# Kernel tuning notes

Measured on AMD Instinct MI355X. Metric: run time of the kernel, lower is better.

Reference implementation:

```python
import jax, jax.numpy as jnp
import numpy as np

N_NODES = 100000
N_TYPES = 7
N_EDGES = 400000
D = 128


def setup_inputs() -> dict:
    key = jax.random.key(0)
    k1, k2, k3, k4 = jax.random.split(key, 4)
    x = jax.random.normal(k1, (N_NODES, D), dtype=jnp.float32)
    edge_indices = jax.random.randint(k2, (N_TYPES, 2, N_EDGES), 0, N_NODES, dtype=jnp.int64)
    # per-type linear weights of the cloned base GNNs (scaled for stability)
    W = jax.random.normal(k3, (N_TYPES, D, D), dtype=jnp.float32) * (1.0 / np.sqrt(D))
    b = jax.random.normal(k4, (N_TYPES, D), dtype=jnp.float32) * 0.02
    return {"x": x, "edge_indices": edge_indices, "W": W, "b": b}


def _type_conv(x, src, dst, Wt, bt, n_nodes):
    # gather -> segment-mean aggregate -> linear, one edge type
    msg = x[src]                                                   # [E, D]
    summed = jax.ops.segment_sum(msg, dst, num_segments=n_nodes)   # [N, D]
    cnt = jax.ops.segment_sum(jnp.ones(src.shape, x.dtype), dst, num_segments=n_nodes)
    mean = summed / jnp.maximum(cnt, 1.0)[:, None]
    return mean @ Wt + bt


def reference(x, edge_indices, W, b):
    n_nodes = x.shape[0]
    n_types = edge_indices.shape[0]
    # loop over the small fixed set of edge types (structurally distinct GNNs)
    acc = jnp.zeros_like(x)
    for t in range(n_types):
        acc = acc + _type_conv(x, edge_indices[t, 0], edge_indices[t, 1], W[t], b[t], n_nodes)
    return acc / n_types
```

## Files before the change

### kernel.cpp

```cpp
#include <hip/hip_runtime.h>

#define N_NODES 100000
#define N_TYPES 7
#define N_EDGES 400000
#define DIM 128
#define NTOT (N_TYPES * N_NODES)
#define ETOT (N_TYPES * N_EDGES)

#define RBITS 10
#define RNODE 1024
#define NBUCK 98
#define NTB (N_TYPES * NBUCK)
#define BSTRIDE 128
#define CAP 6144
#define CHUNK 2048
#define NCHUNKS ((N_EDGES + CHUNK - 1) / CHUNK)

typedef short v8s __attribute__((ext_vector_type(8)));
typedef float v4f __attribute__((ext_vector_type(4)));

__device__ __forceinline__ unsigned short f2bf(float f) {
    unsigned int x = __float_as_uint(f);
    return (unsigned short)((x + 0x7FFFu + ((x >> 16) & 1u)) >> 16);
}

__global__ __launch_bounds__(256) void cast_x_kernel(
    const float* __restrict__ x, unsigned short* __restrict__ xb)
{
    int i = blockIdx.x * 256 + threadIdx.x;
    if (i >= N_NODES * DIM / 4) return;
    float4 v = reinterpret_cast<const float4*>(x)[i];
    ushort4 o;
    o.x = f2bf(v.x); o.y = f2bf(v.y); o.z = f2bf(v.z); o.w = f2bf(v.w);
    reinterpret_cast<ushort4*>(xb)[i] = o;
}

__global__ __launch_bounds__(256) void cast_wt_bsum_kernel(
    const float* __restrict__ W, const float* __restrict__ b,
    unsigned short* __restrict__ WT, float* __restrict__ bsum)
{
    if (blockIdx.x == 448) {
        int j = threadIdx.x;
        if (j < DIM) {
            float s = 0.f;
            for (int t = 0; t < N_TYPES; ++t) s += b[t * DIM + j];
            bsum[j] = s;
        }
        return;
    }
    int i = blockIdx.x * 256 + threadIdx.x;
    if (i >= N_TYPES * DIM * DIM) return;
    int t = i >> 14, r = i & 16383, j = r >> 7, k = r & 127;
    WT[i] = f2bf(W[(t << 14) + (k << 7) + j]);
}

__global__ __launch_bounds__(256) void binpass_kernel(
    const int* __restrict__ ei, int* __restrict__ gcur,
    unsigned int* __restrict__ bucketbuf)
{
    __shared__ unsigned int packedLds[CHUNK];
    __shared__ unsigned char bLds[CHUNK];
    __shared__ unsigned int sortedLds[CHUNK];
    __shared__ int cnt[BSTRIDE];
    __shared__ int lofs[BSTRIDE];
    __shared__ int gbase[BSTRIDE];

    const int blk = blockIdx.x;
    const int t = blk / NCHUNKS;
    const int c = blk - t * NCHUNKS;
    const int* srcp = ei + (size_t)t * 2 * N_EDGES;
    const int* dstp = srcp + N_EDGES;
    const int e0 = c * CHUNK;
    const int e1 = min(e0 + CHUNK, N_EDGES);
    const int tid = threadIdx.x;

    if (tid < BSTRIDE) cnt[tid] = 0;
    __syncthreads();

#pragma unroll
    for (int k = 0; k < CHUNK / 256; ++k) {
        int j = tid + k * 256;
        int e = e0 + j;
        unsigned char b = 0xFF;
        unsigned int pk = 0;
        if (e < e1) {
            int s = srcp[e];
            int d = dstp[e];
            b = (unsigned char)(d >> RBITS);
            pk = ((unsigned int)(d & (RNODE - 1)) << 17) | (unsigned int)s;
            atomicAdd(&cnt[b], 1);
        }
        packedLds[j] = pk;
        bLds[j] = b;
    }
    __syncthreads();

    if (tid < BSTRIDE) lofs[tid] = cnt[tid];
    __syncthreads();
    for (int off = 1; off < BSTRIDE; off <<= 1) {
        int tv = 0;
        if (tid >= off && tid < BSTRIDE) tv = lofs[tid - off];
        __syncthreads();
        if (tid < BSTRIDE) lofs[tid] += tv;
        __syncthreads();
    }
    if (tid < BSTRIDE) lofs[tid] -= cnt[tid];
    __syncthreads();

    if (tid < BSTRIDE) {
        int n = cnt[tid];
        int base = -1;
        if (n > 0 && tid < NBUCK) {
            int rel = atomicAdd(&gcur[t * BSTRIDE + tid], n);
            base = (t * BSTRIDE + tid) * CAP + rel;
        }
        gbase[tid] = base;
        cnt[tid] = lofs[tid];
    }
    __syncthreads();

#pragma unroll
    for (int k = 0; k < CHUNK / 256; ++k) {
        int j = tid + k * 256;
        unsigned char b = bLds[j];
        if (b != 0xFF) {
            int p = atomicAdd(&cnt[b], 1);
            sortedLds[p] = packedLds[j];
        }
    }
    __syncthreads();

    const int wave = tid >> 6, lane = tid & 63;
    for (int b = wave * 32; b < wave * 32 + 32; ++b) {
        if (b >= NBUCK) break;
        int base = gbase[b];
        if (base < 0) continue;
        int o = lofs[b];
        int n = cnt[b] - o;
        for (int i = lane; i < n; i += 64)
            bucketbuf[(size_t)base + i] = sortedLds[o + i];
    }
}

__global__ __launch_bounds__(1024) void bucket_base_kernel(
    const int* __restrict__ gcur, int* __restrict__ sbase, int* __restrict__ offs)
{
    __shared__ int s[1024];
    int tid = threadIdx.x;
    int v = 0;
    if (tid < NTB) {
        int t = tid / NBUCK, b = tid - t * NBUCK;
        v = min(gcur[t * BSTRIDE + b], CAP);
    }
    s[tid] = v;
    __syncthreads();
    for (int off = 1; off < 1024; off <<= 1) {
        int t2 = (tid >= off) ? s[tid - off] : 0;
        __syncthreads();
        s[tid] += t2;
        __syncthreads();
    }
    if (tid < NTB) sbase[tid] = s[tid] - v;
    if (tid == 0) offs[NTOT] = ETOT;
}

__global__ __launch_bounds__(256) void hist_place_kernel(
    const unsigned int* __restrict__ bucketbuf, const int* __restrict__ gcur,
    const int* __restrict__ sbase,
    int* __restrict__ offs, int* __restrict__ srcperm)
{
    __shared__ unsigned int sorted[CAP];
    __shared__ unsigned int sorted2[CAP];
    __shared__ int cnt[RNODE];
    __shared__ int s[256];

    const int blk = blockIdx.x;
    const int t = blk / NBUCK;
    const int b = blk - t * NBUCK;
    const int n = min(gcur[t * BSTRIDE + b], CAP);
    const int ebase = sbase[blk];
    const int g0 = b << RBITS;
    const int validR = min(RNODE, N_NODES - g0);
    const int tid = threadIdx.x;

    const unsigned int* bb = bucketbuf + (size_t)(t * BSTRIDE + b) * CAP;
    for (int i = tid; i < n; i += 256) sorted[i] = bb[i];
    for (int j = tid; j < RNODE; j += 256) cnt[j] = 0;
    __syncthreads();

    for (int i = tid; i < n; i += 256)
        atomicAdd(&cnt[sorted[i] >> 17], 1);
    __syncthreads();

    int base4 = tid * 4;
    int v[4], tot = 0;
#pragma unroll
    for (int k = 0; k < 4; ++k) { v[k] = cnt[base4 + k]; tot += v[k]; }
    s[tid] = tot;
    __syncthreads();
    for (int off = 1; off < 256; off <<= 1) {
        int t2 = (tid >= off) ? s[tid - off] : 0;
        __syncthreads();
        s[tid] += t2;
        __syncthreads();
    }
    int run = s[tid] - tot;
    int* og = offs + (size_t)t * N_NODES + g0;
#pragma unroll
    for (int k = 0; k < 4; ++k) {
        if (base4 + k < validR) og[base4 + k] = ebase + run;
        cnt[base4 + k] = run;
        run += v[k];
    }
    __syncthreads();

    for (int i = tid; i < n; i += 256) {
        unsigned int pk = sorted[i];
        int p = atomicAdd(&cnt[pk >> 17], 1);
        sorted2[p] = pk & 0x1FFFFu;
    }
    __syncthreads();

    int* outp = srcperm + ebase;
    for (int i = tid; i < n; i += 256) outp[i] = (int)sorted2[i];
}

__global__ __launch_bounds__(256) void aggregate_kernel(
    const unsigned short* __restrict__ xb,
    const int* __restrict__ offs,
    const int* __restrict__ srcperm,
    unsigned short* __restrict__ meanout,
    int grp0, int ngrp)
{
    int gi = blockIdx.x * 16 + (threadIdx.x >> 4);
    if (gi >= ngrp) return;
    int grp = grp0 + gi;
    int l = threadIdx.x & 15;

    int beg = offs[grp];
    int end = offs[grp + 1];
    int m = end - beg;

    int mm = m;
    mm = max(mm, __shfl_xor(mm, 16));
    mm = max(mm, __shfl_xor(mm, 32));

    float a[8];
#pragma unroll
    for (int j = 0; j < 8; ++j) a[j] = 0.f;

    const int eSafe = min(beg, ETOT - 1);
#pragma unroll 4
    for (int i = 0; i < mm; ++i) {
        bool valid = i < m;
        int e = valid ? (beg + i) : eSafe;
        int s = srcperm[e];
        uint4 v = *reinterpret_cast<const uint4*>(
            reinterpret_cast<const char*>(xb) + ((size_t)s << 8) + (l << 4));
        float w = valid ? 1.f : 0.f;
        a[0] += w * __uint_as_float(v.x << 16);
        a[1] += w * __uint_as_float(v.x & 0xFFFF0000u);
        a[2] += w * __uint_as_float(v.y << 16);
        a[3] += w * __uint_as_float(v.y & 0xFFFF0000u);
        a[4] += w * __uint_as_float(v.z << 16);
        a[5] += w * __uint_as_float(v.z & 0xFFFF0000u);
        a[6] += w * __uint_as_float(v.w << 16);
        a[7] += w * __uint_as_float(v.w & 0xFFFF0000u);
    }

    float inv = 1.0f / fmaxf((float)m, 1.0f);
    unsigned int p0, p1, p2, p3;
    asm("v_cvt_pk_bf16_f32 %0, %1, %2" : "=v"(p0) : "v"(a[0] * inv), "v"(a[1] * inv));
    asm("v_cvt_pk_bf16_f32 %0, %1, %2" : "=v"(p1) : "v"(a[2] * inv), "v"(a[3] * inv));
    asm("v_cvt_pk_bf16_f32 %0, %1, %2" : "=v"(p2) : "v"(a[4] * inv), "v"(a[5] * inv));
    asm("v_cvt_pk_bf16_f32 %0, %1, %2" : "=v"(p3) : "v"(a[6] * inv), "v"(a[7] * inv));
    uint4 o = make_uint4(p0, p1, p2, p3);
    *reinterpret_cast<uint4*>(
        reinterpret_cast<char*>(meanout) + ((size_t)gi << 8) + (l << 4)) = o;
}

__global__ __launch_bounds__(256) void matmul_kernel(
    const unsigned short* __restrict__ meanall, size_t meanStride,
    int t0, int nt,
    const unsigned short* __restrict__ WT,
    const float* __restrict__ bsum,
    float* __restrict__ out, int accum)
{
    __shared__ unsigned short sB[DIM * DIM];

    const int tid = threadIdx.x;
    const int wave = tid >> 6;
    const int lane = tid & 63;
    const int rlo = lane & 15;
    const int khi = lane >> 4;
    const int row0 = blockIdx.x * 128 + wave * 16;

    v4f acc[2][8];
#pragma unroll
    for (int u = 0; u < 2; ++u)
#pragma unroll
        for (int n = 0; n < 8; ++n) acc[u][n] = (v4f){0.f, 0.f, 0.f, 0.f};

    int rowA0 = row0 + rlo;       if (rowA0 >= N_NODES) rowA0 = N_NODES - 1;
    int rowA1 = row0 + 64 + rlo;  if (rowA1 >= N_NODES) rowA1 = N_NODES - 1;

    for (int tt = 0; tt < nt; ++tt) {
        int t = t0 + tt;
        __syncthreads();
        const uint4* gw = reinterpret_cast<const uint4*>(WT + ((size_t)t << 14));
#pragma unroll
        for (int i = 0; i < 8; ++i) {
            int c = tid + (i << 8);
            uint4 v = gw[c];
            int L = c << 4;
            int row = L >> 8;
            int sb = (row << 8) | ((L & 255) ^ ((row & 7) << 4));
            *reinterpret_cast<uint4*>(reinterpret_cast<char*>(sB) + sb) = v;
        }
        __syncthreads();

        const unsigned short* ar0 = meanall + (size_t)tt * meanStride + ((size_t)rowA0 << 7);
        const unsigned short* ar1 = meanall + (size_t)tt * meanStride + ((size_t)rowA1 << 7);

#pragma unroll
        for (int k0 = 0; k0 < DIM; k0 += 32) {
            v8s a0 = *reinterpret_cast<const v8s*>(ar0 + k0 + (khi << 3));
            v8s a1 = *reinterpret_cast<const v8s*>(ar1 + k0 + (khi << 3));
#pragma unroll
            for (int n = 0; n < 8; ++n) {
                int jrow = (n << 4) | rlo;
                int kb = (k0 + (khi << 3)) << 1;
                int sb = (jrow << 8) | (kb ^ ((jrow & 7) << 4));
                v8s bf = *reinterpret_cast<const v8s*>(reinterpret_cast<char*>(sB) + sb);
                acc[0][n] = __builtin_amdgcn_mfma_f32_16x16x32_bf16(a0, bf, acc[0][n], 0, 0, 0);
                acc[1][n] = __builtin_amdgcn_mfma_f32_16x16x32_bf16(a1, bf, acc[1][n], 0, 0, 0);
            }
        }
    }

    const float inv7 = 1.0f / 7.0f;
#pragma unroll
    for (int u = 0; u < 2; ++u) {
#pragma unroll
        for (int n = 0; n < 8; ++n) {
            int col = (n << 4) | rlo;
            float bs = bsum[col];
#pragma unroll
            for (int r = 0; r < 4; ++r) {
                int row = row0 + u * 64 + (khi << 2) + r;
                if (row < N_NODES) {
                    float* p = out + ((size_t)row << 7) + col;
                    if (accum) *p += acc[u][n][r] * inv7;
                    else       *p = (acc[u][n][r] + bs) * inv7;
                }
            }
        }
    }
}

__global__ __launch_bounds__(256) void out_init_kernel(
    const float* __restrict__ bsum, float* __restrict__ out)
{
    int i = blockIdx.x * 256 + threadIdx.x;
    if (i >= N_NODES * DIM / 4) return;
    int c4 = (i & 31) * 4;
    const float inv7 = 1.0f / 7.0f;
    float4 bv = *reinterpret_cast<const float4*>(bsum + c4);
    float4 o = make_float4(bv.x * inv7, bv.y * inv7, bv.z * inv7, bv.w * inv7);
    reinterpret_cast<float4*>(out)[i] = o;
}

extern "C" void kernel_launch(void* const* d_in, const int* in_sizes, int n_in,
                              void* d_out, int out_size, void* d_ws, size_t ws_size,
                              hipStream_t stream) {
    const float* x  = (const float*)d_in[0];
    const int*   ei = (const int*)d_in[1];
    const float* W  = (const float*)d_in[2];
    const float* b  = (const float*)d_in[3];
    float* out = (float*)d_out;

    char* p = (char*)d_ws;
    unsigned short* xb = (unsigned short*)p;          p += (size_t)N_NODES * DIM * 2;
    unsigned short* WT = (unsigned short*)p;          p += (size_t)N_TYPES * DIM * DIM * 2;
    float* bsum = (float*)p;                          p += 512;
    int* srcperm = (int*)p;                           p += (size_t)ETOT * 4;
    int* offs = (int*)p;                              p += (size_t)(NTOT + 1) * 4;
    int* sbase = (int*)p;                             p += 1024 * 4;
    int* gcur = (int*)p;                              p += (size_t)N_TYPES * BSTRIDE * 4;
    p = (char*)(((uintptr_t)p + 15) & ~(uintptr_t)15);
    unsigned int* bucketbuf = (unsigned int*)p;
    unsigned short* meanbuf = (unsigned short*)p;
    size_t mean1_bytes = (size_t)N_NODES * DIM * 2;
    size_t used = (size_t)(p - (char*)d_ws);
    size_t bucket_bytes = (size_t)N_TYPES * BSTRIDE * CAP * 4;
    bool fused = (ws_size >= used + 7 * mean1_bytes) &&
                 (7 * mean1_bytes >= bucket_bytes);

    cast_x_kernel<<<(N_NODES * DIM / 4 + 255) / 256, 256, 0, stream>>>(x, xb);
    cast_wt_bsum_kernel<<<449, 256, 0, stream>>>(W, b, WT, bsum);

    hipMemsetAsync(gcur, 0, (size_t)N_TYPES * BSTRIDE * 4, stream);
    binpass_kernel<<<N_TYPES * NCHUNKS, 256, 0, stream>>>(ei, gcur, bucketbuf);
    bucket_base_kernel<<<1, 1024, 0, stream>>>(gcur, sbase, offs);
    hist_place_kernel<<<NTB, 256, 0, stream>>>(bucketbuf, gcur, sbase, offs, srcperm);

    const int matmul_blocks = (N_NODES + 127) / 128;

    if (fused) {
        size_t meanStride = (size_t)N_NODES * DIM;
        aggregate_kernel<<<(NTOT + 15) / 16, 256, 0, stream>>>(
            xb, offs, srcperm, meanbuf, 0, NTOT);
        matmul_kernel<<<matmul_blocks, 256, 0, stream>>>(
            meanbuf, meanStride, 0, N_TYPES, WT, bsum, out, 0);
    } else {
        out_init_kernel<<<(N_NODES * DIM / 4 + 255) / 256, 256, 0, stream>>>(bsum, out);
        for (int t = 0; t < N_TYPES; ++t) {
            aggregate_kernel<<<(N_NODES + 15) / 16, 256, 0, stream>>>(
                xb, offs, srcperm, meanbuf, t * N_NODES, N_NODES);
            matmul_kernel<<<matmul_blocks, 256, 0, stream>>>(
                meanbuf, 0, t, 1, WT, bsum, out, 1);
        }
    }
}
```

Baseline: 246.0 us.

## Merge prep kernels and memset, fold bucket prefix scan into placement kernel

Combines the x cast, weight transpose-cast, bias sum and gcur zeroing into a single prep kernel, replacing two kernels and a memset. The separate single-block bucket_base scan is removed: each hist_place block now reduces the counts of all earlier buckets itself to get its base offset. CAP is lowered so the two shared sorted buffers use less LDS, which may let more blocks run per CU but drops edges silently if a bucket ever holds more than the new capacity. Each placement block now does redundant reads of up to ~686 counters.

Result: faster. 232.0 us (-5.7%).

```diff
diff --git a/kernel.cpp b/kernel.cpp
--- a/kernel.cpp
+++ b/kernel.cpp
@@ -12,7 +12,7 @@
 #define NBUCK 98
 #define NTB (N_TYPES * NBUCK)
 #define BSTRIDE 128
-#define CAP 6144
+#define CAP 4992
 #define CHUNK 2048
 #define NCHUNKS ((N_EDGES + CHUNK - 1) / CHUNK)
 
@@ -24,34 +24,41 @@
     return (unsigned short)((x + 0x7FFFu + ((x >> 16) & 1u)) >> 16);
 }
 
-__global__ __launch_bounds__(256) void cast_x_kernel(
-    const float* __restrict__ x, unsigned short* __restrict__ xb)
-{
-    int i = blockIdx.x * 256 + threadIdx.x;
-    if (i >= N_NODES * DIM / 4) return;
-    float4 v = reinterpret_cast<const float4*>(x)[i];
-    ushort4 o;
-    o.x = f2bf(v.x); o.y = f2bf(v.y); o.z = f2bf(v.z); o.w = f2bf(v.w);
-    reinterpret_cast<ushort4*>(xb)[i] = o;
-}
-
-__global__ __launch_bounds__(256) void cast_wt_bsum_kernel(
-    const float* __restrict__ W, const float* __restrict__ b,
-    unsigned short* __restrict__ WT, float* __restrict__ bsum)
-{
-    if (blockIdx.x == 448) {
-        int j = threadIdx.x;
-        if (j < DIM) {
+#define XBLOCKS 12500
+__global__ __launch_bounds__(256) void prep_kernel(
+    const float* __restrict__ x, const float* __restrict__ W,
+    const float* __restrict__ b,
+    unsigned short* __restrict__ xb, unsigned short* __restrict__ WT,
+    float* __restrict__ bsum, int* __restrict__ gcur)
+{
+    int blk = blockIdx.x;
+    if (blk < XBLOCKS) {
+        int i = blk * 256 + threadIdx.x;
+        if (i >= N_NODES * DIM / 4) return;
+        float4 v = reinterpret_cast<const float4*>(x)[i];
+        ushort4 o;
+        o.x = f2bf(v.x); o.y = f2bf(v.y); o.z = f2bf(v.z); o.w = f2bf(v.w);
+        reinterpret_cast<ushort4*>(xb)[i] = o;
+        return;
+    }
+    int j = blk - XBLOCKS;
+    if (j < 448) {
+        int i = j * 256 + threadIdx.x;
+        if (i >= N_TYPES * DIM * DIM) return;
+        int t = i >> 14, r = i & 16383, jj = r >> 7, k = r & 127;
+        WT[i] = f2bf(W[(t << 14) + (k << 7) + jj]);
+        return;
+    }
+    if (j == 448) {
+        int c = threadIdx.x;
+        if (c < DIM) {
             float s = 0.f;
-            for (int t = 0; t < N_TYPES; ++t) s += b[t * DIM + j];
-            bsum[j] = s;
+            for (int t = 0; t < N_TYPES; ++t) s += b[t * DIM + c];
+            bsum[c] = s;
         }
         return;
     }
-    int i = blockIdx.x * 256 + threadIdx.x;
-    if (i >= N_TYPES * DIM * DIM) return;
-    int t = i >> 14, r = i & 16383, j = r >> 7, k = r & 127;
-    WT[i] = f2bf(W[(t << 14) + (k << 7) + j]);
+    for (int i = threadIdx.x; i < N_TYPES * BSTRIDE; i += 256) gcur[i] = 0;
 }
 
 __global__ __launch_bounds__(256) void binpass_kernel(
@@ -142,49 +149,44 @@
     }
 }
 
-__global__ __launch_bounds__(1024) void bucket_base_kernel(
-    const int* __restrict__ gcur, int* __restrict__ sbase, int* __restrict__ offs)
-{
-    __shared__ int s[1024];
-    int tid = threadIdx.x;
-    int v = 0;
-    if (tid < NTB) {
-        int t = tid / NBUCK, b = tid - t * NBUCK;
-        v = min(gcur[t * BSTRIDE + b], CAP);
-    }
-    s[tid] = v;
-    __syncthreads();
-    for (int off = 1; off < 1024; off <<= 1) {
-        int t2 = (tid >= off) ? s[tid - off] : 0;
-        __syncthreads();
-        s[tid] += t2;
-        __syncthreads();
-    }
-    if (tid < NTB) sbase[tid] = s[tid] - v;
-    if (tid == 0) offs[NTOT] = ETOT;
-}
-
 __global__ __launch_bounds__(256) void hist_place_kernel(
     const unsigned int* __restrict__ bucketbuf, const int* __restrict__ gcur,
-    const int* __restrict__ sbase,
     int* __restrict__ offs, int* __restrict__ srcperm)
 {
     __shared__ unsigned int sorted[CAP];
     __shared__ unsigned int sorted2[CAP];
     __shared__ int cnt[RNODE];
     __shared__ int s[256];
+    __shared__ int ebaseS;
 
     const int blk = blockIdx.x;
     const int t = blk / NBUCK;
     const int b = blk - t * NBUCK;
     const int n = min(gcur[t * BSTRIDE + b], CAP);
-    const int ebase = sbase[blk];
     const int g0 = b << RBITS;
     const int validR = min(RNODE, N_NODES - g0);
     const int tid = threadIdx.x;
 
-    const unsigned int* bb = bucketbuf + (size_t)(t * BSTRIDE + b) * CAP;
-    for (int i = tid; i < n; i += 256) sorted[i] = bb[i];
+    {
+        int partial = 0;
+        for (int i = tid; i < blk; i += 256) {
+            int tt = i / NBUCK, bb = i - tt * NBUCK;
+            partial += min(gcur[tt * BSTRIDE + bb], CAP);
+        }
+        s[tid] = partial;
+        __syncthreads();
+        for (int off = 128; off > 0; off >>= 1) {
+            if (tid < off) s[tid] += s[tid + off];
+            __syncthreads();
+        }
+        if (tid == 0) ebaseS = s[0];
+        __syncthreads();
+    }
+    const int ebase = ebaseS;
+    if (blk == 0 && tid == 0) offs[NTOT] = ETOT;
+
+    const unsigned int* bb2 = bucketbuf + (size_t)(t * BSTRIDE + b) * CAP;
+    for (int i = tid; i < n; i += 256) sorted[i] = bb2[i];
     for (int j = tid; j < RNODE; j += 256) cnt[j] = 0;
     __syncthreads();
 
@@ -385,7 +387,6 @@
     float* bsum = (float*)p;                          p += 512;
     int* srcperm = (int*)p;                           p += (size_t)ETOT * 4;
     int* offs = (int*)p;                              p += (size_t)(NTOT + 1) * 4;
-    int* sbase = (int*)p;                             p += 1024 * 4;
     int* gcur = (int*)p;                              p += (size_t)N_TYPES * BSTRIDE * 4;
     p = (char*)(((uintptr_t)p + 15) & ~(uintptr_t)15);
     unsigned int* bucketbuf = (unsigned int*)p;
@@ -396,13 +397,9 @@
     bool fused = (ws_size >= used + 7 * mean1_bytes) &&
                  (7 * mean1_bytes >= bucket_bytes);
 
-    cast_x_kernel<<<(N_NODES * DIM / 4 + 255) / 256, 256, 0, stream>>>(x, xb);
-    cast_wt_bsum_kernel<<<449, 256, 0, stream>>>(W, b, WT, bsum);
-
-    hipMemsetAsync(gcur, 0, (size_t)N_TYPES * BSTRIDE * 4, stream);
+    prep_kernel<<<XBLOCKS + 448 + 2, 256, 0, stream>>>(x, W, b, xb, WT, bsum, gcur);
     binpass_kernel<<<N_TYPES * NCHUNKS, 256, 0, stream>>>(ei, gcur, bucketbuf);
-    bucket_base_kernel<<<1, 1024, 0, stream>>>(gcur, sbase, offs);
-    hist_place_kernel<<<NTB, 256, 0, stream>>>(bucketbuf, gcur, sbase, offs, srcperm);
+    hist_place_kernel<<<NTB, 256, 0, stream>>>(bucketbuf, gcur, offs, srcperm);
 
     const int matmul_blocks = (N_NODES + 127) / 128;
 
```
